# Optimization experiments

Hardware: AMD Instinct MI355X
Metric: run time of the kernel (lower is better)

## Reference

```python
import jax, jax.numpy as jnp
import numpy as np


def setup_inputs() -> dict:
    key = jax.random.key(0)
    k1, k2 = jax.random.split(key)
    B, C, H, W = 8, 64, 128, 512
    image_tensor = jax.random.normal(k1, (B, C, H, W), dtype=jnp.float32)
    # positive metric depths in ~[1, 56] m
    depth = jax.random.uniform(k2, (B, H, W), dtype=jnp.float32) * 55.0 + 1.0
    fx = fy = 500.0; cx = 512.0; cy = 128.0  # intrinsics for original 1024x256 image
    camera_k = jnp.tile(jnp.array([[fx, 0.0, cx], [0.0, fy, cy], [0.0, 0.0, 1.0]],
                                  dtype=jnp.float32)[None], (B, 1, 1))
    meter_per_pixel = jnp.full((1,), 0.25, dtype=jnp.float32)
    return {"image_tensor": image_tensor, "camera_k": camera_k, "depth": depth,
            "meter_per_pixel": meter_per_pixel, "sat_width": 512,
            "ori_grdH": 256, "ori_grdW": 1024}


def reference(image_tensor, camera_k, depth, meter_per_pixel, sat_width, ori_grdH, ori_grdW):
    B, C, H, W = image_tensor.shape
    half = sat_width // 2
    mpp = meter_per_pixel.reshape(())

    # scale intrinsics from original image size to feature-map size (rows 0 and 1)
    row_scale = jnp.array([W / ori_grdW, H / ori_grdH, 1.0], dtype=jnp.float32)
    ck = camera_k * row_scale[None, :, None]
    k_inv = jnp.linalg.inv(ck)  # [B,3,3]

    # back-project pixel grid: xyz_w[b,h,w,:] = K^-1 @ [u,v,1]
    v, u = jnp.meshgrid(jnp.arange(H, dtype=jnp.float32),
                        jnp.arange(W, dtype=jnp.float32), indexing='ij')
    uv1 = jnp.stack([u, v, jnp.ones_like(u)], axis=-1)          # [H,W,3]
    xyz_w = jnp.einsum('bij,hwj->bhwi', k_inv, uv1)             # [B,H,W,3]
    # depth is already at (H,W): bilinear same-size resize is identity
    xyz = (xyz_w * depth[..., None] * 1.2).reshape(B * H * W, 3)

    feats = image_tensor.transpose(0, 2, 3, 1).reshape(B * H * W, C)

    # voxelize x,z (torch .long() truncates toward zero)
    x = jnp.trunc(xyz[:, 0] / mpp).astype(jnp.int32)
    z = jnp.trunc(xyz[:, 2] / mpp).astype(jnp.int32)
    y = xyz[:, 1]
    b = jnp.repeat(jnp.arange(B, dtype=jnp.int32), H * W)

    kept = (x >= -half) & (x <= half - 1) & (z >= -half) & (z <= half - 1)
    max_h = jnp.max(jnp.where(kept, y, -jnp.inf))
    xx = x + half
    zz = z + half
    h = max_h - y  # height key; the last entry per voxel (max h) survives dedup

    # voxel rank (same encoding as torch); out-of-bounds points get a sentinel
    rank0 = zz * (sat_width * B) + (xx + 1) * B + b
    SENT = sat_width * sat_width * B + B
    rank0 = jnp.where(kept, rank0, SENT)

    # torch: sort by h, then stable sort by rank0  == lexsort(primary=rank0, secondary=h)
    order = jnp.lexsort((h, rank0))
    r_s = rank0[order]
    f_s = feats[order]
    b_s, xx_s, zz_s = b[order], xx[order], zz[order]

    # keep the last point of each rank0 group (highest h in that voxel)
    is_last = jnp.concatenate([r_s[:-1] != r_s[1:], jnp.array([True])])
    valid = is_last & (r_s != SENT)

    flat = b_s * (sat_width * sat_width) + xx_s * sat_width + zz_s
    flat = jnp.where(valid, flat, B * sat_width * sat_width)  # invalid -> OOB, dropped

    final = jnp.zeros((B * sat_width * sat_width, C), dtype=jnp.float32)
    final = final.at[flat].set(f_s, mode='drop')
    return final.reshape(B, sat_width, sat_width, C).transpose(0, 3, 1, 2)
```

## Files before the change

kernel.cpp:

```cpp
#include <hip/hip_runtime.h>

#define BB 8
#define CC 64
#define HH 128
#define WW 512
#define SS 512
#define HALF 256
#define HWP (HH * WW)
#define BHW (BB * HWP)
#define CELLS (BB * SS * SS)

__device__ __forceinline__ unsigned int order_f32(float f) {
    unsigned int u = __float_as_uint(f);
    return (u & 0x80000000u) ? ~u : (u | 0x80000000u);
}

__global__ __launch_bounds__(256) void proj_kernel(
    const float* __restrict__ camera_k,
    const float* __restrict__ depth,
    const float* __restrict__ mpp_p,
    unsigned long long* __restrict__ keys)
{
    __shared__ float sk[9];
    const int idx = blockIdx.x * 256 + threadIdx.x;
    const int b = idx >> 16;

    if (threadIdx.x == 0) {
        const float rs[3] = {0.5f, 0.5f, 1.0f};
        double a[9];
        #pragma unroll
        for (int i = 0; i < 3; ++i)
            #pragma unroll
            for (int j = 0; j < 3; ++j)
                a[i*3 + j] = (double)__fmul_rn(camera_k[b*9 + i*3 + j], rs[i]);
        double det = a[0]*(a[4]*a[8]-a[5]*a[7])
                   - a[1]*(a[3]*a[8]-a[5]*a[6])
                   + a[2]*(a[3]*a[7]-a[4]*a[6]);
        double inv[9];
        inv[0] =  (a[4]*a[8]-a[5]*a[7])/det;
        inv[1] = -(a[1]*a[8]-a[2]*a[7])/det;
        inv[2] =  (a[1]*a[5]-a[2]*a[4])/det;
        inv[3] = -(a[3]*a[8]-a[5]*a[6])/det;
        inv[4] =  (a[0]*a[8]-a[2]*a[6])/det;
        inv[5] = -(a[0]*a[5]-a[2]*a[3])/det;
        inv[6] =  (a[3]*a[7]-a[4]*a[6])/det;
        inv[7] = -(a[0]*a[7]-a[1]*a[6])/det;
        inv[8] =  (a[0]*a[4]-a[1]*a[3])/det;
        #pragma unroll
        for (int i = 0; i < 9; ++i) sk[i] = (float)inv[i];
    }
    __syncthreads();

    const int rem = idx & (HWP - 1);
    const int v = rem >> 9;
    const int u = rem & (WW - 1);
    const float d = depth[idx];
    const float mpp = mpp_p[0];
    const float uf = (float)u, vf = (float)v;

    float xw = __fadd_rn(__fadd_rn(__fmul_rn(sk[0], uf), __fmul_rn(sk[1], vf)), sk[2]);
    float yw = __fadd_rn(__fadd_rn(__fmul_rn(sk[3], uf), __fmul_rn(sk[4], vf)), sk[5]);
    float zw = __fadd_rn(__fadd_rn(__fmul_rn(sk[6], uf), __fmul_rn(sk[7], vf)), sk[8]);
    float x3 = __fmul_rn(__fmul_rn(xw, d), 1.2f);
    float y3 = __fmul_rn(__fmul_rn(yw, d), 1.2f);
    float z3 = __fmul_rn(__fmul_rn(zw, d), 1.2f);

    int xi = (int)truncf(__fdiv_rn(x3, mpp));
    int zi = (int)truncf(__fdiv_rn(z3, mpp));

    if (xi >= -HALF && xi <= HALF - 1 && zi >= -HALF && zi <= HALF - 1) {
        int cell = (b << 18) | ((xi + HALF) << 9) | (zi + HALF);
        unsigned long long key =
            ((unsigned long long)order_f32(y3) << 32) | (unsigned int)(~idx);
        atomicMin(&keys[cell], key);
    }
}

__global__ __launch_bounds__(256) void scatter_kernel(
    const float* __restrict__ img,
    const unsigned long long* __restrict__ keys,
    float* __restrict__ out)
{
    const int q     = blockIdx.x * 256 + threadIdx.x;
    const int c0    = blockIdx.y << 2;
    const int cell0 = q << 2;
    const int b     = cell0 >> 18;
    const int local = cell0 & (SS * SS - 1);

    const ulonglong2* kp = (const ulonglong2*)keys + (size_t)q * 2;
    const ulonglong2 ka = kp[0];
    const ulonglong2 kb = kp[1];
    const unsigned long long k[4] = {ka.x, ka.y, kb.x, kb.y};

    int  rem[4];
    bool has[4];
    #pragma unroll
    for (int i = 0; i < 4; ++i) {
        has[i] = (k[i] != ~0ull);
        rem[i] = (int)((~(unsigned int)(k[i] & 0xFFFFFFFFull)) & (HWP - 1));
    }

    const float* plane0 = img + ((size_t)(b * CC + c0)) * HWP;
    float*       op     = out + ((size_t)(b * CC + c0)) * (size_t)(SS * SS) + local;

    float v[4][4];
    #pragma unroll
    for (int c = 0; c < 4; ++c) {
        const float* pl = plane0 + (size_t)c * HWP;
        #pragma unroll
        for (int i = 0; i < 4; ++i)
            v[c][i] = has[i] ? pl[rem[i]] : 0.0f;
    }
    #pragma unroll
    for (int c = 0; c < 4; ++c) {
        float4 f4 = make_float4(v[c][0], v[c][1], v[c][2], v[c][3]);
        *(float4*)(op + (size_t)c * (SS * SS)) = f4;
    }
}

extern "C" void kernel_launch(void* const* d_in, const int* in_sizes, int n_in,
                              void* d_out, int out_size, void* d_ws, size_t ws_size,
                              hipStream_t stream) {
    const float* img      = (const float*)d_in[0];
    const float* camera_k = (const float*)d_in[1];
    const float* depth    = (const float*)d_in[2];
    const float* mpp      = (const float*)d_in[3];

    unsigned long long* keys = (unsigned long long*)d_ws;

    hipMemsetAsync(keys, 0xFF, (size_t)CELLS * sizeof(unsigned long long), stream);

    proj_kernel<<<BHW / 256, 256, 0, stream>>>(camera_k, depth, mpp, keys);

    dim3 sgrid(CELLS / 4 / 256, CC / 4);
    scatter_kernel<<<sgrid, 256, 0, stream>>>(img, keys, (float*)d_out);
}
```

Measured before the change: 796.5 us.

## Pack winner keys into 32-bit indices and widen scatter channel groups

Adds a pack kernel that turns the 64-bit atomic keys into 32-bit source indices with a sentinel for empty cells. The scatter kernel then reads these compact indices and handles 8 channels per thread instead of 4. It also reorders the grid so the 8 channel groups of one cell block sit in consecutive blocks, and writes the output with nontemporal stores. The goal is less key traffic to the scatter, which previously re-read the 64-bit keys for every channel group, plus better cache locality. The cost is one extra kernel launch and one extra pass over the keys.

```diff
diff --git a/kernel.cpp b/kernel.cpp
--- a/kernel.cpp
+++ b/kernel.cpp
@@ -9,6 +9,8 @@
 #define HWP (HH * WW)
 #define BHW (BB * HWP)
 #define CELLS (BB * SS * SS)
+
+typedef float vfloat4 __attribute__((ext_vector_type(4)));
 
 __device__ __forceinline__ unsigned int order_f32(float f) {
     unsigned int u = __float_as_uint(f);
@@ -76,45 +78,51 @@
     }
 }
 
+__global__ __launch_bounds__(256) void pack_kernel(
+    const unsigned long long* __restrict__ keys,
+    unsigned int* __restrict__ win)
+{
+    const int i = blockIdx.x * 256 + threadIdx.x;
+    ulonglong2 k = ((const ulonglong2*)keys)[i];
+    uint2 o;
+    o.x = (k.x != ~0ull) ? ((~(unsigned int)k.x) & (HWP - 1)) : 0xFFFFFFFFu;
+    o.y = (k.y != ~0ull) ? ((~(unsigned int)k.y) & (HWP - 1)) : 0xFFFFFFFFu;
+    ((uint2*)win)[i] = o;
+}
+
 __global__ __launch_bounds__(256) void scatter_kernel(
     const float* __restrict__ img,
-    const unsigned long long* __restrict__ keys,
+    const unsigned int* __restrict__ win,
     float* __restrict__ out)
 {
-    const int q     = blockIdx.x * 256 + threadIdx.x;
-    const int c0    = blockIdx.y << 2;
+    const int n  = blockIdx.x;
+    const int sg = n & 7;
+    const int qb = n >> 3;
+
+    const int q     = qb * 256 + threadIdx.x;
+    const int c0    = sg << 3;
     const int cell0 = q << 2;
     const int b     = cell0 >> 18;
     const int local = cell0 & (SS * SS - 1);
 
-    const ulonglong2* kp = (const ulonglong2*)keys + (size_t)q * 2;
-    const ulonglong2 ka = kp[0];
-    const ulonglong2 kb = kp[1];
-    const unsigned long long k[4] = {ka.x, ka.y, kb.x, kb.y};
-
-    int  rem[4];
-    bool has[4];
-    #pragma unroll
-    for (int i = 0; i < 4; ++i) {
-        has[i] = (k[i] != ~0ull);
-        rem[i] = (int)((~(unsigned int)(k[i] & 0xFFFFFFFFull)) & (HWP - 1));
-    }
+    const uint4 w = ((const uint4*)win)[q];
+    const unsigned int wv[4] = {w.x, w.y, w.z, w.w};
 
     const float* plane0 = img + ((size_t)(b * CC + c0)) * HWP;
     float*       op     = out + ((size_t)(b * CC + c0)) * (size_t)(SS * SS) + local;
 
-    float v[4][4];
+    float v[8][4];
     #pragma unroll
-    for (int c = 0; c < 4; ++c) {
+    for (int c = 0; c < 8; ++c) {
         const float* pl = plane0 + (size_t)c * HWP;
         #pragma unroll
         for (int i = 0; i < 4; ++i)
-            v[c][i] = has[i] ? pl[rem[i]] : 0.0f;
+            v[c][i] = (wv[i] != 0xFFFFFFFFu) ? pl[wv[i]] : 0.0f;
     }
     #pragma unroll
-    for (int c = 0; c < 4; ++c) {
-        float4 f4 = make_float4(v[c][0], v[c][1], v[c][2], v[c][3]);
-        *(float4*)(op + (size_t)c * (SS * SS)) = f4;
+    for (int c = 0; c < 8; ++c) {
+        vfloat4 f4 = {v[c][0], v[c][1], v[c][2], v[c][3]};
+        __builtin_nontemporal_store(f4, (vfloat4*)(op + (size_t)c * (SS * SS)));
     }
 }
 
@@ -127,11 +135,12 @@
     const float* mpp      = (const float*)d_in[3];
 
     unsigned long long* keys = (unsigned long long*)d_ws;
+    unsigned int*       win  = (unsigned int*)((char*)d_ws + (size_t)CELLS * 8);
 
-    hipMemsetAsync(keys, 0xFF, (size_t)CELLS * sizeof(unsigned long long), stream);
+    (void)hipMemsetAsync(keys, 0xFF, (size_t)CELLS * sizeof(unsigned long long), stream);
 
     proj_kernel<<<BHW / 256, 256, 0, stream>>>(camera_k, depth, mpp, keys);
+    pack_kernel<<<CELLS / 2 / 256, 256, 0, stream>>>(keys, win);
 
-    dim3 sgrid(CELLS / 4 / 256, CC / 4);
-    scatter_kernel<<<sgrid, 256, 0, stream>>>(img, keys, (float*)d_out);
+    scatter_kernel<<<16384, 256, 0, stream>>>(img, win, (float*)d_out);
 }
```

New measurement: 765.2 us. 1.04x faster.
